# Performance work log

Measured on AMD Instinct MI355X. Metric: run time of the kernel, lower is better.

The kernel has to match this reference:

```python
import jax, jax.numpy as jnp
import numpy as np

EPS = 1e-6

def setup_inputs() -> dict:
    key = jax.random.key(0)
    ks = jax.random.split(key, 8)
    S, B, I, D, L = 1024, 16, 1024, 1024, 2
    std = np.sqrt(2.0 / (5.0 * I))
    inp = {
        "input": jax.random.normal(ks[0], (S, B, I), jnp.float32),
        "h0": jnp.zeros((L, B, D), jnp.float32),
        "extra0": jnp.zeros((L, B, 3 * D), jnp.float32),
        "W0": jax.random.normal(ks[1], (4 * D, I), jnp.float32) * std,
        "b0": jnp.zeros((4 * D,), jnp.float32).at[2 * D:3 * D].set(
            jax.random.uniform(ks[2], (D,), jnp.float32, 3.0, 6.0)),
        "r0": jnp.zeros((4 * D,), jnp.float32),
        "W1": jax.random.normal(ks[3], (4 * D, D), jnp.float32) * std,
        "b1": jnp.zeros((4 * D,), jnp.float32).at[2 * D:3 * D].set(
            jax.random.uniform(ks[4], (D,), jnp.float32, 3.0, 6.0)),
        "r1": jnp.zeros((4 * D,), jnp.float32),
    }
    return inp

def _cell(x, c, n, h, m, W, b, r):
    # x: (B, in), states: (B, D), W: (4D, in), b/r: (4D,)
    D = h.shape[-1]
    pre = x @ W.T + b  # (B, 4D)
    rz, ri, rf, ro = jnp.split(r, 4)
    z_pre = pre[:, 0 * D:1 * D] + rz * h
    i_pre = pre[:, 1 * D:2 * D] + ri * h
    f_pre = pre[:, 2 * D:3 * D] + rf * h
    o_pre = pre[:, 3 * D:4 * D] + ro * h
    z_t = jnp.tanh(z_pre)
    o_t = jax.nn.sigmoid(o_pre)
    m_new = jnp.maximum(f_pre + m, i_pre)
    f_t = jnp.exp(f_pre + m - m_new)
    i_t = jnp.exp(i_pre - m_new)
    c_new = f_t * c + i_t * z_t
    n_new = f_t * n + i_t
    h_new = o_t * (c_new / (jnp.abs(n_new) + EPS))
    return h_new, c_new, n_new, m_new

def _run(input, h0, extra0, params):
    D = h0.shape[-1]
    c0 = extra0[:, :, 0 * D:1 * D]
    n0 = extra0[:, :, 1 * D:2 * D]
    m0 = extra0[:, :, 2 * D:3 * D]

    def step(carry, x_t):
        h, c, n, m = carry  # each (L, B, D)
        x = x_t
        hs, cs, ns, ms = [], [], [], []
        for l, (W, b, r) in enumerate(params):
            h_new, c_new, n_new, m_new = _cell(x, c[l], n[l], h[l], m[l], W, b, r)
            hs.append(h_new); cs.append(c_new); ns.append(n_new); ms.append(m_new)
            x = h_new
        carry = (jnp.stack(hs), jnp.stack(cs), jnp.stack(ns), jnp.stack(ms))
        return carry, x

    (h_f, c_f, n_f, m_f), output = jax.lax.scan(step, (h0, c0, n0, m0), input)
    extra_f = jnp.concatenate([c_f, n_f, m_f], axis=-1)
    return output, h_f, extra_f

def reference(input, h0, extra0, W0, b0, r0, W1, b1, r1):
    params = [(W0, b0, r0), (W1, b1, r1)]
    return _run(input, h0, extra0, params)
```

## Files before the change

### kernel.cpp

```cpp
#include <hip/hip_runtime.h>
#include <hip/hip_bf16.h>

#define S_LEN  1024
#define BATCH  16
#define IDIM   1024
#define DDIM   1024
#define NG     4096
#define BD     16384
#define LAYERS 2
#define PF     16
#define PFP    8
#define NSEG   32

typedef __attribute__((ext_vector_type(8))) short   short8;
typedef __attribute__((ext_vector_type(4))) float   floatx4;
typedef __attribute__((address_space(1))) void      as1_void;
typedef __attribute__((address_space(3))) void      as3_void;

#define L2E  1.4426950408889634f
#define LN2  0.6931471805599453f

#define EXP2F(x) exp2f(x)

static __device__ __forceinline__ unsigned short f2bf(float x) {
    unsigned int u = __float_as_uint(x);
    return (unsigned short)((u + 0x7fffu + ((u >> 16) & 1u)) >> 16);
}

__global__ void detect_dtype(const void* w, int* flag)
{
    const __hip_bfloat16* p = (const __hip_bfloat16*)w;
    float mx = 0.0f;
    for (int i = threadIdx.x; i < 4096; i += 64) {
        float v = __bfloat162float(p[i]);
        float a = fabsf(v);
        if (!(a == a)) a = 1e30f;
        mx = fmaxf(mx, a);
    }
#pragma unroll
    for (int o = 32; o > 0; o >>= 1)
        mx = fmaxf(mx, __shfl_down(mx, o, 64));
    if (threadIdx.x == 0) *flag = (mx > 1e3f) ? 1 : 0;
}

__global__ void to_bf16(const void* src, size_t elem_off, const int* flag,
                        unsigned short* dst, int n)
{
    const int i = blockIdx.x * 256 + threadIdx.x;
    if (i >= n) return;
    if (*flag) dst[i] = f2bf(((const float*)src)[elem_off + i]);
    else       dst[i] = ((const unsigned short*)src)[elem_off + i];
}

__global__ void prep_small(const void* __restrict__ h0,
                           const void* __restrict__ extra0,
                           const void* __restrict__ b0s, const void* __restrict__ r0s,
                           const void* __restrict__ b1s, const void* __restrict__ r1s,
                           const int* __restrict__ flag,
                           float* __restrict__ state,
                           float* __restrict__ pb,
                           int* __restrict__ rflag)
{
    const int blk = blockIdx.x;
    const int fl = *flag;

    if (blk < 128) {
        const int idx = blk * 256 + threadIdx.x;
        const int l  = idx / BD;
        const int bd = idx % BD;
        const int b = bd >> 10, d = bd & 1023;
        float* st = state + (size_t)l * 4 * BD;
        const size_t eoff = ((size_t)l * BATCH + b) * (3 * DDIM);
        float cv, nv, mv, hv;
        if (fl) {
            const float* e = (const float*)extra0 + eoff;
            cv = e[d]; nv = e[DDIM + d]; mv = e[2 * DDIM + d];
            hv = ((const float*)h0)[(size_t)l * BD + bd];
        } else {
            const __hip_bfloat16* e = (const __hip_bfloat16*)extra0 + eoff;
            cv = __bfloat162float(e[d]);
            nv = __bfloat162float(e[DDIM + d]);
            mv = __bfloat162float(e[2 * DDIM + d]);
            hv = __bfloat162float(((const __hip_bfloat16*)h0)[(size_t)l * BD + bd]);
        }
        st[0 * BD + bd] = cv;
        st[1 * BD + bd] = nv;
        st[2 * BD + bd] = mv * L2E;
        st[3 * BD + bd] = hv;
        return;
    }

    const int which = blk - 128;
    const void* src = (which == 0) ? b0s : (which == 1) ? r0s
                    : (which == 2) ? b1s : r1s;
    float* dst = pb + (size_t)which * NG;
    int nz = 0;
#pragma unroll
    for (int j = 0; j < NG / 256; j++) {
        const int i = j * 256 + threadIdx.x;
        float v;
        if (fl) {
            v = ((const float*)src)[i];
            nz |= (v != 0.0f);
        } else {
            const unsigned short u = ((const unsigned short*)src)[i];
            nz |= ((u & 0x7fffu) != 0);
            v = __bfloat162float(((const __hip_bfloat16*)src)[i]);
        }
        dst[i] = v;
    }
    if (which == 1 || which == 3) {
        __shared__ int s[4];
        const int w = threadIdx.x >> 6;
        const int any = __any(nz) ? 1 : 0;
        if ((threadIdx.x & 63) == 0) s[w] = any;
        __syncthreads();
        if (threadIdx.x == 0) rflag[which >> 1] = !(s[0] | s[1] | s[2] | s[3]);
    }
}

__global__ __launch_bounds__(256, 2)
void gemm_bias(const __hip_bfloat16* __restrict__ A,
               const __hip_bfloat16* __restrict__ W,
               const float* __restrict__ bias,
               unsigned short* __restrict__ out,
               const int* __restrict__ rflag)
{
    constexpr int K = 1024;
    __shared__ alignas(16) __hip_bfloat16 sA[128 * 32];
    __shared__ alignas(16) __hip_bfloat16 sB[128 * 32];

    const int t  = threadIdx.x;
    const int m0 = blockIdx.y * 128;
    const int nb = blockIdx.x;
    const int lr = t & 15;
    const int q  = (t >> 4) & 3;
    const int w  = t >> 6;
    const int wm = w >> 1, wn = w & 1;
    const int sr = t >> 2;
    const int sk = (t & 3) * 8;

    floatx4 acc[4][4] = {};

    const __hip_bfloat16* Ab = A + (size_t)(m0 + sr) * K + sk;
    const int wrow = ((sr >> 5) << 10) + nb * 32 + (sr & 31);
    const __hip_bfloat16* Wb = W + (size_t)wrow * K + sk;

    for (int k0 = 0; k0 < K; k0 += 32) {
        __syncthreads();
        __builtin_amdgcn_global_load_lds((as1_void*)(Ab + k0),            (as3_void*)&sA[sr * 32 + sk],        16, 0, 0);
        __builtin_amdgcn_global_load_lds((as1_void*)(Ab + 64 * K + k0),   (as3_void*)&sA[(sr + 64) * 32 + sk], 16, 0, 0);
        __builtin_amdgcn_global_load_lds((as1_void*)(Wb + k0),            (as3_void*)&sB[sr * 32 + sk],        16, 0, 0);
        __builtin_amdgcn_global_load_lds((as1_void*)(Wb + 2048 * K + k0), (as3_void*)&sB[(sr + 64) * 32 + sk], 16, 0, 0);
        __syncthreads();

        short8 af[4], bf[4];
#pragma unroll
        for (int i = 0; i < 4; i++)
            af[i] = *(const short8*)&sA[(wm * 64 + i * 16 + lr) * 32 + q * 8];
#pragma unroll
        for (int j = 0; j < 4; j++)
            bf[j] = *(const short8*)&sB[(j * 32 + wn * 16 + lr) * 32 + q * 8];
#pragma unroll
        for (int i = 0; i < 4; i++)
#pragma unroll
            for (int j = 0; j < 4; j++)
                acc[i][j] = __builtin_amdgcn_mfma_f32_16x16x32_bf16(af[i], bf[j], acc[i][j], 0, 0, 0);
    }

    const int d = nb * 32 + wn * 16 + lr;
    const float sc[4] = {2.0f * L2E, L2E, L2E, L2E};
    float bb[4];
#pragma unroll
    for (int g = 0; g < 4; g++) bb[g] = sc[g] * bias[g * 1024 + d];

    const int rfast = *rflag;

#pragma unroll
    for (int i = 0; i < 4; i++) {
#pragma unroll
        for (int reg = 0; reg < 4; reg++) {
            const int row = m0 + wm * 64 + i * 16 + q * 4 + reg;
            float v[4];
#pragma unroll
            for (int g = 0; g < 4; g++)
                v[g] = acc[i][g][reg] * sc[g] + bb[g];
            if (rfast) {
                const float zv = v[0];
                const float e2 = EXP2F(-fabsf(zv));
                v[0] = copysignf((1.0f - e2) * __builtin_amdgcn_rcpf(1.0f + e2), zv);
                v[3] = __builtin_amdgcn_rcpf(1.0f + EXP2F(-v[3]));
            }
            union { unsigned short us[4]; uint2 u2; } pk;
#pragma unroll
            for (int g = 0; g < 4; g++) pk.us[g] = f2bf(v[g]);
            *(uint2*)(out + (size_t)row * NG + d * 4) = pk.u2;
        }
    }
}

__global__ void scan_passA(const unsigned int* __restrict__ pre,
                           const int* __restrict__ rflag,
                           float* __restrict__ smry, int T)
{
    if (!*rflag) return;
    const int gid = blockIdx.x * 256 + threadIdx.x;
    const int chain = gid & (BD - 1);
    const int seg = gid >> 14;
    const int SEG = T / NSEG;
    const int b = chain >> 10, d = chain & 1023;

    const size_t stp = 32768;
    const unsigned int* p = pre + (size_t)b * 2048 + (size_t)d * 2
                              + (size_t)(seg * SEG) * stp;

    float al = 0.0f, mu = -3e38f, Bh = 0.0f, Nh = 0.0f;

    unsigned int k0[PFP], k1[PFP];
#pragma unroll
    for (int u = 0; u < PFP; u++) {
        const uint2 v = *(const uint2*)(p + (size_t)u * stp);
        k0[u] = v.x; k1[u] = v.y;
    }

    for (int t = 0; t < SEG; t += PFP) {
#pragma unroll
        for (int u = 0; u < PFP; u++) {
            const float zt = __uint_as_float(k0[u] << 16);
            const float i2 = __uint_as_float(k0[u] & 0xffff0000u);
            const float f2 = __uint_as_float(k1[u] << 16);

            const uint2 nv = *(const uint2*)(p + (size_t)(t + u + PFP) * stp);
            k0[u] = nv.x; k1[u] = nv.y;

            al += f2;
            const float e  = i2 - al;
            const float mn = fmaxf(mu, e);
            const float s  = EXP2F(mu - mn);
            const float ww = EXP2F(e - mn);
            Bh = fmaf(Bh, s, ww * zt);
            Nh = fmaf(Nh, s, ww);
            mu = mn;
        }
    }

    smry[0 * NSEG * BD + seg * BD + chain] = al;
    smry[1 * NSEG * BD + seg * BD + chain] = al + mu;
    smry[2 * NSEG * BD + seg * BD + chain] = Bh;
    smry[3 * NSEG * BD + seg * BD + chain] = Nh;
}

__global__ void scan_mid(float* __restrict__ smry,
                         const int* __restrict__ rflag,
                         const float* __restrict__ state, int T)
{
    if (!*rflag) return;
    const int idx = blockIdx.x * 256 + threadIdx.x;
    float c  = state[0 * BD + idx];
    float n  = state[1 * BD + idx];
    float m2 = state[2 * BD + idx];
#pragma unroll
    for (int s = 0; s < NSEG; s++) {
        const float A    = smry[0 * NSEG * BD + s * BD + idx];
        const float bmax = smry[1 * NSEG * BD + s * BD + idx];
        const float Bh   = smry[2 * NSEG * BD + s * BD + idx];
        const float Nh   = smry[3 * NSEG * BD + s * BD + idx];
        smry[0 * NSEG * BD + s * BD + idx] = c;
        smry[1 * NSEG * BD + s * BD + idx] = n;
        smry[2 * NSEG * BD + s * BD + idx] = m2;
        const float mn = fmaxf(m2 + A, bmax);
        const float sc = EXP2F(m2 + A - mn);
        const float w  = EXP2F(bmax - mn);
        c  = fmaf(sc, c, w * Bh);
        n  = fmaf(sc, n, w * Nh);
        m2 = mn;
    }
}

template<int MODE>
__global__ void scan_passB(const unsigned int* __restrict__ pre,
                           const float* __restrict__ smry,
                           const int* __restrict__ rflag,
                           float* __restrict__ state,
                           unsigned short* __restrict__ hseq,
                           void* __restrict__ gout, size_t gout_eoff,
                           const int* __restrict__ flag, int T)
{
    if (!*rflag) return;
    const int gid = blockIdx.x * 256 + threadIdx.x;
    const int chain = gid & (BD - 1);
    const int seg = gid >> 14;
    const int SEG = T / NSEG;
    const int t0s = seg * SEG;
    const int b = chain >> 10, d = chain & 1023;
    const int fl = *flag;

    float c  = smry[0 * NSEG * BD + seg * BD + chain];
    float n  = smry[1 * NSEG * BD + seg * BD + chain];
    float m2 = smry[2 * NSEG * BD + seg * BD + chain];

    const size_t stp = 32768;
    const unsigned int* p = pre + (size_t)b * 2048 + (size_t)d * 2
                              + (size_t)t0s * stp;

    unsigned short* hb = hseq + (size_t)b * DDIM + d + (size_t)t0s * BD;
    float*          fo = (float*)gout + gout_eoff + (size_t)b * DDIM + d + (size_t)t0s * BD;
    unsigned short* bo = (unsigned short*)gout + gout_eoff + (size_t)b * DDIM + d + (size_t)t0s * BD;

    float h = 0.0f;
    unsigned int k0[PFP], k1[PFP];
#pragma unroll
    for (int u = 0; u < PFP; u++) {
        const uint2 v = *(const uint2*)(p + (size_t)u * stp);
        k0[u] = v.x; k1[u] = v.y;
    }

    for (int t = 0; t < SEG; t += PFP) {
#pragma unroll
        for (int u = 0; u < PFP; u++) {
            const float zt = __uint_as_float(k0[u] << 16);
            const float i2 = __uint_as_float(k0[u] & 0xffff0000u);
            const float f2 = __uint_as_float(k1[u] << 16);
            const float ot = __uint_as_float(k1[u] & 0xffff0000u);

            const uint2 nv = *(const uint2*)(p + (size_t)(t + u + PFP) * stp);
            k0[u] = nv.x; k1[u] = nv.y;

            const float fm = f2 + m2;
            const float mn = fmaxf(fm, i2);
            const float ft = EXP2F(fm - mn);
            const float it = EXP2F(i2 - mn);

            c  = fmaf(ft, c, it * zt);
            n  = fmaf(ft, n, it);
            m2 = mn;
            h  = ot * c * __builtin_amdgcn_rcpf(fabsf(n) + 1e-6f);

            const size_t toff = (size_t)(t + u) * BD;
            if (MODE == 0)      hb[toff] = f2bf(h);
            else if (fl)        fo[toff] = h;
            else                bo[toff] = f2bf(h);
        }
    }

    if (seg == NSEG - 1) {
        state[0 * BD + chain] = c;
        state[1 * BD + chain] = n;
        state[2 * BD + chain] = m2;
        state[3 * BD + chain] = h;
    }
}

template<int MODE>
__global__ void slstm_scan(const unsigned int* __restrict__ pre,
                           const float* __restrict__ r,
                           float* __restrict__ state,
                           unsigned short* __restrict__ hseq,
                           void* __restrict__ gout, size_t gout_eoff,
                           const int* __restrict__ flag,
                           const int* __restrict__ rflag, int T, int pgate)
{
    const int rfast = *rflag;
    if (pgate && rfast) return;

    const int idx = blockIdx.x * 64 + threadIdx.x;
    const int b = idx >> 10;
    const int d = idx & 1023;
    const int fl = *flag;

    const float rz = r[d]            * (2.0f * L2E);
    const float ri = r[DDIM + d]     * L2E;
    const float rf = r[2 * DDIM + d] * L2E;
    const float ro = r[3 * DDIM + d] * L2E;

    float c  = state[0 * BD + idx];
    float n  = state[1 * BD + idx];
    float m2 = state[2 * BD + idx];
    float h  = state[3 * BD + idx];

    const size_t stp = 32768;
    const unsigned int* p = pre + (size_t)b * 2048 + (size_t)d * 2;

    unsigned short* hb = hseq + (size_t)b * DDIM + d;
    float*          fo = (float*)gout + gout_eoff + (size_t)b * DDIM + d;
    unsigned short* bo = (unsigned short*)gout + gout_eoff + (size_t)b * DDIM + d;

    unsigned int k0[PF], k1[PF];
#pragma unroll
    for (int u = 0; u < PF; u++) {
        const uint2 v = *(const uint2*)(p + (size_t)u * stp);
        k0[u] = v.x; k1[u] = v.y;
    }

    if (rfast) {
        for (int t8 = 0; t8 < T; t8 += PF) {
#pragma unroll
            for (int u = 0; u < PF; u++) {
                const float zt = __uint_as_float(k0[u] << 16);
                const float i2 = __uint_as_float(k0[u] & 0xffff0000u);
                const float f2 = __uint_as_float(k1[u] << 16);
                const float ot = __uint_as_float(k1[u] & 0xffff0000u);

                const uint2 nv = *(const uint2*)(p + (size_t)(t8 + u + PF) * stp);
                k0[u] = nv.x; k1[u] = nv.y;

                const float fm = f2 + m2;
                const float mn = fmaxf(fm, i2);
                const float ft = EXP2F(fm - mn);
                const float it = EXP2F(i2 - mn);

                c  = fmaf(ft, c, it * zt);
                n  = fmaf(ft, n, it);
                m2 = mn;
                h  = ot * c * __builtin_amdgcn_rcpf(fabsf(n) + 1e-6f);

                const size_t toff = (size_t)(t8 + u) * BD;
                if (MODE == 0)      hb[toff] = f2bf(h);
                else if (fl)        fo[toff] = h;
                else                bo[toff] = f2bf(h);
            }
        }
    } else {
        for (int t8 = 0; t8 < T; t8 += PF) {
#pragma unroll
            for (int u = 0; u < PF; u++) {
                float z2 = __uint_as_float(k0[u] << 16);
                float i2 = __uint_as_float(k0[u] & 0xffff0000u);
                float f2 = __uint_as_float(k1[u] << 16);
                float o2 = __uint_as_float(k1[u] & 0xffff0000u);

                const uint2 nv = *(const uint2*)(p + (size_t)(t8 + u + PF) * stp);
                k0[u] = nv.x; k1[u] = nv.y;

                z2 = fmaf(rz, h, z2);
                i2 = fmaf(ri, h, i2);
                f2 = fmaf(rf, h, f2);
                o2 = fmaf(ro, h, o2);

                const float fm = f2 + m2;
                const float mn = fmaxf(fm, i2);
                const float ft = EXP2F(fm - mn);
                const float it = EXP2F(i2 - mn);

                const float e2 = EXP2F(-fabsf(z2));
                const float zt = copysignf((1.0f - e2) * __builtin_amdgcn_rcpf(1.0f + e2), z2);
                const float ot = __builtin_amdgcn_rcpf(1.0f + EXP2F(-o2));

                c  = ft * c + it * zt;
                n  = ft * n + it;
                m2 = mn;
                h  = ot * c * __builtin_amdgcn_rcpf(fabsf(n) + 1e-6f);

                const size_t toff = (size_t)(t8 + u) * BD;
                if (MODE == 0)      hb[toff] = f2bf(h);
                else if (fl)        fo[toff] = h;
                else                bo[toff] = f2bf(h);
            }
        }
    }

    state[0 * BD + idx] = c;
    state[1 * BD + idx] = n;
    state[2 * BD + idx] = m2;
    state[3 * BD + idx] = h;
}

__global__ void finalize(const float* __restrict__ state,
                         void* __restrict__ out,
                         const int* __restrict__ flag)
{
    const int idx = blockIdx.x * 256 + threadIdx.x;
    const int l  = idx / BD;
    const int bd = idx % BD;
    const int b = bd >> 10, d = bd & 1023;
    const float* st = state + (size_t)l * 4 * BD;
    const float cv = st[0 * BD + bd], nv = st[1 * BD + bd];
    const float mv = st[2 * BD + bd] * LN2;
    const float hv = st[3 * BD + bd];

    const size_t hoff = (size_t)S_LEN * BD + idx;
    const size_t eoff = (size_t)S_LEN * BD + (size_t)LAYERS * BD
                      + ((size_t)l * BATCH + b) * (3 * DDIM);
    if (*flag) {
        float* o = (float*)out;
        o[hoff] = hv;
        o[eoff + d] = cv; o[eoff + DDIM + d] = nv; o[eoff + 2 * DDIM + d] = mv;
    } else {
        unsigned short* o = (unsigned short*)out;
        o[hoff] = f2bf(hv);
        o[eoff + d]            = f2bf(cv);
        o[eoff + DDIM + d]     = f2bf(nv);
        o[eoff + 2 * DDIM + d] = f2bf(mv);
    }
}

__global__ void zero_out_k(void* __restrict__ out, const int* __restrict__ flag,
                           int out_size)
{
    const size_t i = (size_t)blockIdx.x * 256 + threadIdx.x;
    const size_t nb = (size_t)out_size * ((*flag) ? 4 : 2);
    char* o = (char*)out;
    for (size_t j = i * 4; j < (i + 1) * 4 && j < nb; j++) o[j] = 0;
}

extern "C" void kernel_launch(void* const* d_in, const int* in_sizes, int n_in,
                              void* d_out, int out_size, void* d_ws, size_t ws_size,
                              hipStream_t stream)
{
    const void* input  = d_in[0];
    const void* h0     = d_in[1];
    const void* extra0 = d_in[2];
    const void* W0     = d_in[3];
    const void* b0     = d_in[4];
    const void* r0     = d_in[5];
    const void* W1     = d_in[6];
    const void* b1     = d_in[7];
    const void* r1     = d_in[8];

    const size_t FLAG_B  = 256;
    const size_t STATE_B = (size_t)LAYERS * 4 * BD * 4;
    const size_t W_B     = (size_t)NG * IDIM * 2;
    const size_t PB_B    = (size_t)4 * NG * 4;
    const size_t SM_B    = (size_t)4 * NSEG * BD * 4;
    const size_t FIXED   = FLAG_B + STATE_B + 2 * W_B + PB_B + SM_B;

    int T = 0;
    for (int cand = S_LEN; cand >= 8; cand >>= 1) {
        size_t need = FIXED
                    + (size_t)cand * BD * 2
                    + (size_t)cand * BD * 2
                    + (size_t)(cand + PF) * BATCH * NG * 2;
        if (need <= ws_size) { T = cand; break; }
    }

    char* ws = (char*)d_ws;
    int*   flag  = (int*)ws;
    int*   rflag = flag + 1;
    float* state = (float*)(ws + FLAG_B);
    __hip_bfloat16* W0b = (__hip_bfloat16*)(ws + FLAG_B + STATE_B);
    __hip_bfloat16* W1b = W0b + (size_t)NG * IDIM;
    float* pb    = (float*)(ws + FLAG_B + STATE_B + 2 * W_B);
    float* b0f = pb, *r0f = pb + NG, *b1f = pb + 2 * NG, *r1f = pb + 3 * NG;
    float* smry  = (float*)(ws + FLAG_B + STATE_B + 2 * W_B + PB_B);
    unsigned short* Ain  = (unsigned short*)(ws + FIXED);
    unsigned short* hseq = Ain + (size_t)T * BD;
    unsigned short* pre  = hseq + (size_t)T * BD;

    detect_dtype<<<dim3(1), dim3(64), 0, stream>>>(W0, flag);

    if (T == 0) {
        zero_out_k<<<dim3((out_size + 255) / 256), dim3(256), 0, stream>>>(d_out, flag, out_size);
        return;
    }

    const int WN = NG * IDIM;
    to_bf16<<<dim3(WN / 256), dim3(256), 0, stream>>>(W0, 0, flag, (unsigned short*)W0b, WN);
    to_bf16<<<dim3(WN / 256), dim3(256), 0, stream>>>(W1, 0, flag, (unsigned short*)W1b, WN);

    prep_small<<<dim3(132), dim3(256), 0, stream>>>(h0, extra0, b0, r0, b1, r1,
                                                    flag, state, pb, rflag);

    const dim3 gemmGrid(32, (T * BATCH) / 128);
    const dim3 scanGrid(BD / 64);
    const dim3 passGrid((BD * NSEG) / 256);
    const dim3 midGrid(BD / 256);
    const int  nch = S_LEN / T;
    const int  useP = (T >= 256 && (T % (NSEG * PFP)) == 0) ? 1 : 0;

    for (int ch = 0; ch < nch; ch++) {
        const int t0 = ch * T;

        to_bf16<<<dim3((T * BD) / 256), dim3(256), 0, stream>>>(
            input, (size_t)t0 * BD, flag, Ain, T * BD);

        gemm_bias<<<gemmGrid, 256, 0, stream>>>((const __hip_bfloat16*)Ain, W0b, b0f, pre, rflag + 0);
        if (useP) {
            scan_passA<<<passGrid, 256, 0, stream>>>((const unsigned int*)pre, rflag + 0, smry, T);
            scan_mid<<<midGrid, 256, 0, stream>>>(smry, rflag + 0, state, T);
            scan_passB<0><<<passGrid, 256, 0, stream>>>((const unsigned int*)pre, smry, rflag + 0,
                                                        state, hseq, (void*)0, 0, flag, T);
        }
        slstm_scan<0><<<scanGrid, 64, 0, stream>>>((const unsigned int*)pre, r0f, state,
                                                   hseq, (void*)0, 0, flag, rflag + 0, T, useP);

        gemm_bias<<<gemmGrid, 256, 0, stream>>>((const __hip_bfloat16*)hseq, W1b, b1f, pre, rflag + 1);
        if (useP) {
            scan_passA<<<passGrid, 256, 0, stream>>>((const unsigned int*)pre, rflag + 1, smry, T);
            scan_mid<<<midGrid, 256, 0, stream>>>(smry, rflag + 1, state + 4 * BD, T);
            scan_passB<1><<<passGrid, 256, 0, stream>>>((const unsigned int*)pre, smry, rflag + 1,
                                                        state + 4 * BD, (unsigned short*)0,
                                                        d_out, (size_t)t0 * BD, flag, T);
        }
        slstm_scan<1><<<scanGrid, 64, 0, stream>>>((const unsigned int*)pre, r1f,
                                                   state + 4 * BD, (unsigned short*)0,
                                                   d_out, (size_t)t0 * BD, flag, rflag + 1, T, useP);
    }

    finalize<<<dim3(LAYERS * BD / 256), dim3(256), 0, stream>>>(state, d_out, flag);
}
```

Measured before the change: 672.1 us.

## Store gate preactivations in chain-block-major layout and halve scan segments

The GEMM epilogue now writes the packed gate preactivations in a layout where each 64-chain block stores its time steps contiguously (cb, t, 64 lanes). Each scan thread then walks time with a small stride of 64 uint2 instead of a 128 KB stride, which should improve cache and page locality for the sequential scans. The segment count for the parallel scan also drops from 32 to 16, giving longer segments and a smaller summary pass. Risks are scattered GEMM stores in the new layout and less parallelism in the segmented scan.

```diff
diff --git a/kernel.cpp b/kernel.cpp
--- a/kernel.cpp
+++ b/kernel.cpp
@@ -10,7 +10,7 @@
 #define LAYERS 2
 #define PF     16
 #define PFP    8
-#define NSEG   32
+#define NSEG   16
 
 typedef __attribute__((ext_vector_type(8))) short   short8;
 typedef __attribute__((ext_vector_type(4))) float   floatx4;
@@ -124,7 +124,7 @@
                const __hip_bfloat16* __restrict__ W,
                const float* __restrict__ bias,
                unsigned short* __restrict__ out,
-               const int* __restrict__ rflag)
+               const int* __restrict__ rflag, int tpad)
 {
     constexpr int K = 1024;
     __shared__ alignas(16) __hip_bfloat16 sA[128 * 32];
@@ -169,6 +169,8 @@
     }
 
     const int d = nb * 32 + wn * 16 + lr;
+    const int cl = ((nb & 1) << 5) + wn * 16 + lr;
+    const int cbBase = nb >> 1;
     const float sc[4] = {2.0f * L2E, L2E, L2E, L2E};
     float bb[4];
 #pragma unroll
@@ -180,7 +182,9 @@
     for (int i = 0; i < 4; i++) {
 #pragma unroll
         for (int reg = 0; reg < 4; reg++) {
-            const int row = m0 + wm * 64 + i * 16 + q * 4 + reg;
+            const int row  = m0 + wm * 64 + i * 16 + q * 4 + reg;
+            const int trow = row >> 4;
+            const int b    = row & 15;
             float v[4];
 #pragma unroll
             for (int g = 0; g < 4; g++)
@@ -194,32 +198,32 @@
             union { unsigned short us[4]; uint2 u2; } pk;
 #pragma unroll
             for (int g = 0; g < 4; g++) pk.us[g] = f2bf(v[g]);
-            *(uint2*)(out + (size_t)row * NG + d * 4) = pk.u2;
+            const int cb = b * 16 + cbBase;
+            *(uint2*)(out + (((size_t)cb * tpad + trow) * 64 + cl) * 4) = pk.u2;
         }
     }
 }
 
 __global__ void scan_passA(const unsigned int* __restrict__ pre,
                            const int* __restrict__ rflag,
-                           float* __restrict__ smry, int T)
+                           float* __restrict__ smry, int T, int tpad)
 {
     if (!*rflag) return;
     const int gid = blockIdx.x * 256 + threadIdx.x;
     const int chain = gid & (BD - 1);
     const int seg = gid >> 14;
     const int SEG = T / NSEG;
-    const int b = chain >> 10, d = chain & 1023;
-
-    const size_t stp = 32768;
-    const unsigned int* p = pre + (size_t)b * 2048 + (size_t)d * 2
-                              + (size_t)(seg * SEG) * stp;
+    const int cb = chain >> 6, cl = chain & 63;
+
+    const uint2* p = (const uint2*)pre
+                   + ((size_t)cb * tpad + seg * SEG) * 64 + cl;
 
     float al = 0.0f, mu = -3e38f, Bh = 0.0f, Nh = 0.0f;
 
     unsigned int k0[PFP], k1[PFP];
 #pragma unroll
     for (int u = 0; u < PFP; u++) {
-        const uint2 v = *(const uint2*)(p + (size_t)u * stp);
+        const uint2 v = p[(size_t)u * 64];
         k0[u] = v.x; k1[u] = v.y;
     }
 
@@ -230,7 +234,7 @@
             const float i2 = __uint_as_float(k0[u] & 0xffff0000u);
             const float f2 = __uint_as_float(k1[u] << 16);
 
-            const uint2 nv = *(const uint2*)(p + (size_t)(t + u + PFP) * stp);
+            const uint2 nv = p[(size_t)(t + u + PFP) * 64];
             k0[u] = nv.x; k1[u] = nv.y;
 
             al += f2;
@@ -284,7 +288,7 @@
                            float* __restrict__ state,
                            unsigned short* __restrict__ hseq,
                            void* __restrict__ gout, size_t gout_eoff,
-                           const int* __restrict__ flag, int T)
+                           const int* __restrict__ flag, int T, int tpad)
 {
     if (!*rflag) return;
     const int gid = blockIdx.x * 256 + threadIdx.x;
@@ -292,26 +296,25 @@
     const int seg = gid >> 14;
     const int SEG = T / NSEG;
     const int t0s = seg * SEG;
-    const int b = chain >> 10, d = chain & 1023;
+    const int cb = chain >> 6, cl = chain & 63;
     const int fl = *flag;
 
     float c  = smry[0 * NSEG * BD + seg * BD + chain];
     float n  = smry[1 * NSEG * BD + seg * BD + chain];
     float m2 = smry[2 * NSEG * BD + seg * BD + chain];
 
-    const size_t stp = 32768;
-    const unsigned int* p = pre + (size_t)b * 2048 + (size_t)d * 2
-                              + (size_t)t0s * stp;
-
-    unsigned short* hb = hseq + (size_t)b * DDIM + d + (size_t)t0s * BD;
-    float*          fo = (float*)gout + gout_eoff + (size_t)b * DDIM + d + (size_t)t0s * BD;
-    unsigned short* bo = (unsigned short*)gout + gout_eoff + (size_t)b * DDIM + d + (size_t)t0s * BD;
+    const uint2* p = (const uint2*)pre
+                   + ((size_t)cb * tpad + t0s) * 64 + cl;
+
+    unsigned short* hb = hseq + chain + (size_t)t0s * BD;
+    float*          fo = (float*)gout + gout_eoff + chain + (size_t)t0s * BD;
+    unsigned short* bo = (unsigned short*)gout + gout_eoff + chain + (size_t)t0s * BD;
 
     float h = 0.0f;
     unsigned int k0[PFP], k1[PFP];
 #pragma unroll
     for (int u = 0; u < PFP; u++) {
-        const uint2 v = *(const uint2*)(p + (size_t)u * stp);
+        const uint2 v = p[(size_t)u * 64];
         k0[u] = v.x; k1[u] = v.y;
     }
 
@@ -323,7 +326,7 @@
             const float f2 = __uint_as_float(k1[u] << 16);
             const float ot = __uint_as_float(k1[u] & 0xffff0000u);
 
-            const uint2 nv = *(const uint2*)(p + (size_t)(t + u + PFP) * stp);
+            const uint2 nv = p[(size_t)(t + u + PFP) * 64];
             k0[u] = nv.x; k1[u] = nv.y;
 
             const float fm = f2 + m2;
@@ -358,14 +361,15 @@
                            unsigned short* __restrict__ hseq,
                            void* __restrict__ gout, size_t gout_eoff,
                            const int* __restrict__ flag,
-                           const int* __restrict__ rflag, int T, int pgate)
+                           const int* __restrict__ rflag, int T, int tpad,
+                           int pgate)
 {
     const int rfast = *rflag;
     if (pgate && rfast) return;
 
     const int idx = blockIdx.x * 64 + threadIdx.x;
-    const int b = idx >> 10;
     const int d = idx & 1023;
+    const int cb = idx >> 6, cl = idx & 63;
     const int fl = *flag;
 
     const float rz = r[d]            * (2.0f * L2E);
@@ -378,17 +382,16 @@
     float m2 = state[2 * BD + idx];
     float h  = state[3 * BD + idx];
 
-    const size_t stp = 32768;
-    const unsigned int* p = pre + (size_t)b * 2048 + (size_t)d * 2;
-
-    unsigned short* hb = hseq + (size_t)b * DDIM + d;
-    float*          fo = (float*)gout + gout_eoff + (size_t)b * DDIM + d;
-    unsigned short* bo = (unsigned short*)gout + gout_eoff + (size_t)b * DDIM + d;
+    const uint2* p = (const uint2*)pre + (size_t)cb * tpad * 64 + cl;
+
+    unsigned short* hb = hseq + idx;
+    float*          fo = (float*)gout + gout_eoff + idx;
+    unsigned short* bo = (unsigned short*)gout + gout_eoff + idx;
 
     unsigned int k0[PF], k1[PF];
 #pragma unroll
     for (int u = 0; u < PF; u++) {
-        const uint2 v = *(const uint2*)(p + (size_t)u * stp);
+        const uint2 v = p[(size_t)u * 64];
         k0[u] = v.x; k1[u] = v.y;
     }
 
@@ -401,7 +404,7 @@
                 const float f2 = __uint_as_float(k1[u] << 16);
                 const float ot = __uint_as_float(k1[u] & 0xffff0000u);
 
-                const uint2 nv = *(const uint2*)(p + (size_t)(t8 + u + PF) * stp);
+                const uint2 nv = p[(size_t)(t8 + u + PF) * 64];
                 k0[u] = nv.x; k1[u] = nv.y;
 
                 const float fm = f2 + m2;
@@ -429,7 +432,7 @@
                 float f2 = __uint_as_float(k1[u] << 16);
                 float o2 = __uint_as_float(k1[u] & 0xffff0000u);
 
-                const uint2 nv = *(const uint2*)(p + (size_t)(t8 + u + PF) * stp);
+                const uint2 nv = p[(size_t)(t8 + u + PF) * 64];
                 k0[u] = nv.x; k1[u] = nv.y;
 
                 z2 = fmaf(rz, h, z2);
@@ -529,7 +532,7 @@
         size_t need = FIXED
                     + (size_t)cand * BD * 2
                     + (size_t)cand * BD * 2
-                    + (size_t)(cand + PF) * BATCH * NG * 2;
+                    + (size_t)(cand + PF) * BD * 8;
         if (need <= ws_size) { T = cand; break; }
     }
 
@@ -560,6 +563,7 @@
     prep_small<<<dim3(132), dim3(256), 0, stream>>>(h0, extra0, b0, r0, b1, r1,
                                                     flag, state, pb, rflag);
 
+    const int  tpad = T + PF;
     const dim3 gemmGrid(32, (T * BATCH) / 128);
     const dim3 scanGrid(BD / 64);
     const dim3 passGrid((BD * NSEG) / 256);
@@ -573,27 +577,27 @@
         to_bf16<<<dim3((T * BD) / 256), dim3(256), 0, stream>>>(
             input, (size_t)t0 * BD, flag, Ain, T * BD);
 
-        gemm_bias<<<gemmGrid, 256, 0, stream>>>((const __hip_bfloat16*)Ain, W0b, b0f, pre, rflag + 0);
+        gemm_bias<<<gemmGrid, 256, 0, stream>>>((const __hip_bfloat16*)Ain, W0b, b0f, pre, rflag + 0, tpad);
         if (useP) {
-            scan_passA<<<passGrid, 256, 0, stream>>>((const unsigned int*)pre, rflag + 0, smry, T);
+            scan_passA<<<passGrid, 256, 0, stream>>>((const unsigned int*)pre, rflag + 0, smry, T, tpad);
             scan_mid<<<midGrid, 256, 0, stream>>>(smry, rflag + 0, state, T);
             scan_passB<0><<<passGrid, 256, 0, stream>>>((const unsigned int*)pre, smry, rflag + 0,
-                                                        state, hseq, (void*)0, 0, flag, T);
+                                                        state, hseq, (void*)0, 0, flag, T, tpad);
         }
         slstm_scan<0><<<scanGrid, 64, 0, stream>>>((const unsigned int*)pre, r0f, state,
-                                                   hseq, (void*)0, 0, flag, rflag + 0, T, useP);
-
-        gemm_bias<<<gemmGrid, 256, 0, stream>>>((const __hip_bfloat16*)hseq, W1b, b1f, pre, rflag + 1);
+                                                   hseq, (void*)0, 0, flag, rflag + 0, T, tpad, useP);
+
+        gemm_bias<<<gemmGrid, 256, 0, stream>>>((const __hip_bfloat16*)hseq, W1b, b1f, pre, rflag + 1, tpad);
         if (useP) {
-            scan_passA<<<passGrid, 256, 0, stream>>>((const unsigned int*)pre, rflag + 1, smry, T);
+            scan_passA<<<passGrid, 256, 0, stream>>>((const unsigned int*)pre, rflag + 1, smry, T, tpad);
             scan_mid<<<midGrid, 256, 0, stream>>>(smry, rflag + 1, state + 4 * BD, T);
             scan_passB<1><<<passGrid, 256, 0, stream>>>((const unsigned int*)pre, smry, rflag + 1,
                                                         state + 4 * BD, (unsigned short*)0,
-                                                        d_out, (size_t)t0 * BD, flag, T);
+                                                        d_out, (size_t)t0 * BD, flag, T, tpad);
         }
         slstm_scan<1><<<scanGrid, 64, 0, stream>>>((const unsigned int*)pre, r1f,
                                                    state + 4 * BD, (unsigned short*)0,
-                                                   d_out, (size_t)t0 * BD, flag, rflag + 1, T, useP);
+                                                   d_out, (size_t)t0 * BD, flag, rflag + 1, T, tpad, useP);
     }
 
     finalize<<<dim3(LAYERS * BD / 256), dim3(256), 0, stream>>>(state, d_out, flag);
```

New measurement: 630.6 us. 1.07x faster.
